# Kernel optimization log

Measured on AMD Instinct MI355X. Metric: run time of the kernel, lower is better.

Reference implementation:

```python
import jax, jax.numpy as jnp
import numpy as np

H, N, CH = 256, 64, 1  # heads/features, diagonal state size, channels


def setup_inputs() -> dict:
    key = jax.random.key(0)
    k1, k2, k3 = jax.random.split(key, 3)
    # |A| in (0.5, 0.999) so exp(dtA * l) decays for large l (matches rho*w construction)
    A_abslog = jnp.log(jax.random.uniform(k1, (H, N), dtype=jnp.float32,
                                          minval=0.5, maxval=0.999))
    A_phase = jax.random.uniform(k2, (H, N), dtype=jnp.float32,
                                 minval=-np.pi, maxval=np.pi)
    # C stored as real view of complex (channels, H, N, 2), like torch.view_as_real
    C = jax.random.normal(k3, (CH, H, N, 2), dtype=jnp.float32)
    return {"A_abslog": A_abslog, "A_phase": A_phase, "C": C, "L": 4096}


def reference(A_abslog, A_phase, C, L):
    # A_eigvals = exp(abslog + i*phase), copies=1 so repeat is identity
    A = jnp.exp(A_abslog + 1j * A_phase)            # (H, N) complex64
    dtA = jnp.log(A)                                 # (H, N)
    Cc = C[..., 0] + 1j * C[..., 1]                  # (CH, H, N)
    Cc = Cc * (A - 1.0) / dtA                        # (CH, H, N)
    t = jnp.arange(L, dtype=jnp.float32)             # (L,)
    K = jnp.exp(dtA[:, :, None] * t)                 # (H, N, L) Vandermonde
    K = jnp.einsum('chn,hnl->chl', Cc, K)            # (CH, H, L)
    return 2.0 * K.real
```

## Files before the change

### kernel.cpp

```cpp
#include <hip/hip_runtime.h>
#include <math.h>


typedef _Float16       f16x8 __attribute__((ext_vector_type(8)));
typedef unsigned int   u32x4 __attribute__((ext_vector_type(4)));
typedef float          f32x4 __attribute__((ext_vector_type(4)));

constexpr int H = 256;
constexpr int N = 64;
constexpr int L = 4096;
constexpr int STRIDE = 76;

constexpr unsigned SEL_LO = 0x05040100u;
constexpr unsigned SEL_HI = 0x07060302u;

__global__ __launch_bounds__(512)
void sskdiag_kernel(const float* __restrict__ A_abslog,
                    const float* __restrict__ A_phase,
                    const float* __restrict__ C,
                    float* __restrict__ out)
{
    __shared__ float4   s_t1[N];
    __shared__ float4   s_t2[N];
    __shared__ __align__(16) unsigned s_G[64 * STRIDE];
    __shared__ __align__(16) unsigned s_M[64 * STRIDE];

    const int h   = blockIdx.x;
    const int tid = threadIdx.x;

    if (tid < N) {
        const int n = tid;
        const float al = A_abslog[h * N + n];
        const float ph = A_phase [h * N + n];
        const double md = (double)ph * 0.15915494309189535;
        const float phrev = (float)(md - floor(md));
        const float sp = __builtin_amdgcn_sinf(phrev);
        const float cp = __builtin_amdgcn_cosf(phrev);
        const float m  = __expf(al);
        const float Ar = m * cp, Ai = m * sp;
        const float nr = Ar - 1.0f, ni = Ai;
        const float inv = 1.0f / (al * al + ph * ph);
        const float gr = (nr * al + ni * ph) * inv;
        const float gi = (ni * al - nr * ph) * inv;
        const float cre = C[(h * N + n) * 2 + 0];
        const float cim = C[(h * N + n) * 2 + 1];
        const float Cr = 2.0f * (cre * gr - cim * gi);
        const float Ci = 2.0f * (cre * gi + cim * gr);
        const double m64 = 64.0 * md;
        const float f64a = (float)(m64 - floor(m64));
        const float mg64 = __expf(64.0f * al);
        s_t1[n] = make_float4(al, phrev, Ar, Ai);
        s_t2[n] = make_float4(mg64 * __builtin_amdgcn_cosf(f64a),
                              mg64 * __builtin_amdgcn_sinf(f64a), Cr, Ci);
    }
    __syncthreads();

    {
        const int n = tid & 63, q = tid >> 6;
        const float4 t1 = s_t1[n];
        const float4 t2 = s_t2[n];
        const float al = t1.x, phrev = t1.y;
        const float Ar = t1.z, Ai = t1.w;
        const float Ur = t2.x, Ui = t2.y;
        const float b0 = (float)(8 * q);
        float tg = phrev * b0;  tg -= floorf(tg);
        const float gmag = __expf(al * b0);
        float gre = gmag * __builtin_amdgcn_cosf(tg);
        float gim = gmag * __builtin_amdgcn_sinf(tg);
        const float e0 = (float)(512 * q);
        float tm = phrev * e0;  tm -= floorf(tm);
        const float umag = __expf(al * e0);
        const float ure = umag * __builtin_amdgcn_cosf(tm);
        const float uim = umag * __builtin_amdgcn_sinf(tm);
        float mre = t2.z * ure - t2.w * uim;
        float mim = t2.z * uim + t2.w * ure;

        #pragma unroll
        for (int k = 0; k < 8; ++k) {
            const int row = 8 * q + k;
            union { _Float16 hh[2]; unsigned u; } pg, pm;
            pg.hh[0] = (_Float16)gre;  pg.hh[1] = (_Float16)(-gim);
            pm.hh[0] = (_Float16)mre;  pm.hh[1] = (_Float16)mim;
            s_G[row * STRIDE + n] = pg.u;
            s_M[row * STRIDE + n] = pm.u;
            const float ngr = gre * Ar - gim * Ai;
            gim = gre * Ai + gim * Ar;  gre = ngr;
            const float nmr = mre * Ur - mim * Ui;
            mim = mre * Ui + mim * Ur;  mre = nmr;
        }
    }
    __syncthreads();

    const int w    = tid >> 6;
    const int lane = tid & 63;
    const int e    = lane & 15;
    const int kg   = lane >> 4;
    const int ta   = w >> 1;
    const int tb0  = 2 * (w & 1);

    f16x8 fMr[2], fMi[2];
    #pragma unroll
    for (int s = 0; s < 2; ++s) {
        const unsigned* p = &s_M[(ta * 16 + e) * STRIDE + 32 * s + 8 * kg];
        const u32x4 v0 = *reinterpret_cast<const u32x4*>(p);
        const u32x4 v1 = *reinterpret_cast<const u32x4*>(p + 4);
        u32x4 rr, ii;
        rr[0] = __builtin_amdgcn_perm(v0[1], v0[0], SEL_LO);
        rr[1] = __builtin_amdgcn_perm(v0[3], v0[2], SEL_LO);
        rr[2] = __builtin_amdgcn_perm(v1[1], v1[0], SEL_LO);
        rr[3] = __builtin_amdgcn_perm(v1[3], v1[2], SEL_LO);
        ii[0] = __builtin_amdgcn_perm(v0[1], v0[0], SEL_HI);
        ii[1] = __builtin_amdgcn_perm(v0[3], v0[2], SEL_HI);
        ii[2] = __builtin_amdgcn_perm(v1[1], v1[0], SEL_HI);
        ii[3] = __builtin_amdgcn_perm(v1[3], v1[2], SEL_HI);
        fMr[s] = __builtin_bit_cast(f16x8, rr);
        fMi[s] = __builtin_bit_cast(f16x8, ii);
    }

    #pragma unroll
    for (int t = 0; t < 2; ++t) {
        const int tb = tb0 + t;
        f32x4 acc = {0.f, 0.f, 0.f, 0.f};
        #pragma unroll
        for (int s = 0; s < 2; ++s) {
            const unsigned* p = &s_G[(tb * 16 + e) * STRIDE + 32 * s + 8 * kg];
            const u32x4 v0 = *reinterpret_cast<const u32x4*>(p);
            const u32x4 v1 = *reinterpret_cast<const u32x4*>(p + 4);
            u32x4 rr, ii;
            rr[0] = __builtin_amdgcn_perm(v0[1], v0[0], SEL_LO);
            rr[1] = __builtin_amdgcn_perm(v0[3], v0[2], SEL_LO);
            rr[2] = __builtin_amdgcn_perm(v1[1], v1[0], SEL_LO);
            rr[3] = __builtin_amdgcn_perm(v1[3], v1[2], SEL_LO);
            ii[0] = __builtin_amdgcn_perm(v0[1], v0[0], SEL_HI);
            ii[1] = __builtin_amdgcn_perm(v0[3], v0[2], SEL_HI);
            ii[2] = __builtin_amdgcn_perm(v1[1], v1[0], SEL_HI);
            ii[3] = __builtin_amdgcn_perm(v1[3], v1[2], SEL_HI);
            const f16x8 fGr = __builtin_bit_cast(f16x8, rr);
            const f16x8 fGi = __builtin_bit_cast(f16x8, ii);
            acc = __builtin_amdgcn_mfma_f32_16x16x32_f16(fGr, fMr[s], acc, 0, 0, 0);
            acc = __builtin_amdgcn_mfma_f32_16x16x32_f16(fGi, fMi[s], acc, 0, 0, 0);
        }
        float4 v;
        v.x = acc[0];  v.y = acc[1];  v.z = acc[2];  v.w = acc[3];
        *reinterpret_cast<float4*>(out + h * L + (ta * 16 + e) * 64
                                   + tb * 16 + kg * 4) = v;
    }
}

extern "C" void kernel_launch(void* const* d_in, const int* in_sizes, int n_in,
                              void* d_out, int out_size, void* d_ws, size_t ws_size,
                              hipStream_t stream)
{
    const float* A_abslog = (const float*)d_in[0];
    const float* A_phase  = (const float*)d_in[1];
    const float* C        = (const float*)d_in[2];
    float* out = (float*)d_out;

    sskdiag_kernel<<<H, 512, 0, stream>>>(A_abslog, A_phase, C, out);
}
```

Baseline: 10.97 us.

## Halve block to 256 threads, each wave computing four output tiles

The block shrinks from 8 to 4 waves. Each thread now fills 16 rows of the G/M tables instead of 8. Each wave loads all four G tiles plus one M tile into registers and issues 16 MFMAs over four output tiles. The aim is to cut redundant LDS fragment loads and per-block thread overhead, at the cost of longer serial recurrence chains and fewer waves for latency hiding.

```diff
diff --git a/kernel.cpp b/kernel.cpp
--- a/kernel.cpp
+++ b/kernel.cpp
@@ -14,7 +14,7 @@
 constexpr unsigned SEL_LO = 0x05040100u;
 constexpr unsigned SEL_HI = 0x07060302u;
 
-__global__ __launch_bounds__(512)
+__global__ __launch_bounds__(256)
 void sskdiag_kernel(const float* __restrict__ A_abslog,
                     const float* __restrict__ A_phase,
                     const float* __restrict__ C,
@@ -62,22 +62,22 @@
         const float al = t1.x, phrev = t1.y;
         const float Ar = t1.z, Ai = t1.w;
         const float Ur = t2.x, Ui = t2.y;
-        const float b0 = (float)(8 * q);
+        const float b0 = (float)(16 * q);
         float tg = phrev * b0;  tg -= floorf(tg);
         const float gmag = __expf(al * b0);
         float gre = gmag * __builtin_amdgcn_cosf(tg);
         float gim = gmag * __builtin_amdgcn_sinf(tg);
-        const float e0 = (float)(512 * q);
-        float tm = phrev * e0;  tm -= floorf(tm);
-        const float umag = __expf(al * e0);
+        const float a64 = (float)(1024 * q);
+        float tm = phrev * a64;  tm -= floorf(tm);
+        const float umag = __expf(al * a64);
         const float ure = umag * __builtin_amdgcn_cosf(tm);
         const float uim = umag * __builtin_amdgcn_sinf(tm);
         float mre = t2.z * ure - t2.w * uim;
         float mim = t2.z * uim + t2.w * ure;
 
         #pragma unroll
-        for (int k = 0; k < 8; ++k) {
-            const int row = 8 * q + k;
+        for (int k = 0; k < 16; ++k) {
+            const int row = 16 * q + k;
             union { _Float16 hh[2]; unsigned u; } pg, pm;
             pg.hh[0] = (_Float16)gre;  pg.hh[1] = (_Float16)(-gim);
             pm.hh[0] = (_Float16)mre;  pm.hh[1] = (_Float16)mim;
@@ -95,34 +95,13 @@
     const int lane = tid & 63;
     const int e    = lane & 15;
     const int kg   = lane >> 4;
-    const int ta   = w >> 1;
-    const int tb0  = 2 * (w & 1);
 
-    f16x8 fMr[2], fMi[2];
+    f16x8 fGr[2][4], fGi[2][4], fMr[2], fMi[2];
+
     #pragma unroll
     for (int s = 0; s < 2; ++s) {
-        const unsigned* p = &s_M[(ta * 16 + e) * STRIDE + 32 * s + 8 * kg];
-        const u32x4 v0 = *reinterpret_cast<const u32x4*>(p);
-        const u32x4 v1 = *reinterpret_cast<const u32x4*>(p + 4);
-        u32x4 rr, ii;
-        rr[0] = __builtin_amdgcn_perm(v0[1], v0[0], SEL_LO);
-        rr[1] = __builtin_amdgcn_perm(v0[3], v0[2], SEL_LO);
-        rr[2] = __builtin_amdgcn_perm(v1[1], v1[0], SEL_LO);
-        rr[3] = __builtin_amdgcn_perm(v1[3], v1[2], SEL_LO);
-        ii[0] = __builtin_amdgcn_perm(v0[1], v0[0], SEL_HI);
-        ii[1] = __builtin_amdgcn_perm(v0[3], v0[2], SEL_HI);
-        ii[2] = __builtin_amdgcn_perm(v1[1], v1[0], SEL_HI);
-        ii[3] = __builtin_amdgcn_perm(v1[3], v1[2], SEL_HI);
-        fMr[s] = __builtin_bit_cast(f16x8, rr);
-        fMi[s] = __builtin_bit_cast(f16x8, ii);
-    }
-
-    #pragma unroll
-    for (int t = 0; t < 2; ++t) {
-        const int tb = tb0 + t;
-        f32x4 acc = {0.f, 0.f, 0.f, 0.f};
         #pragma unroll
-        for (int s = 0; s < 2; ++s) {
+        for (int tb = 0; tb < 4; ++tb) {
             const unsigned* p = &s_G[(tb * 16 + e) * STRIDE + 32 * s + 8 * kg];
             const u32x4 v0 = *reinterpret_cast<const u32x4*>(p);
             const u32x4 v1 = *reinterpret_cast<const u32x4*>(p + 4);
@@ -135,15 +114,39 @@
             ii[1] = __builtin_amdgcn_perm(v0[3], v0[2], SEL_HI);
             ii[2] = __builtin_amdgcn_perm(v1[1], v1[0], SEL_HI);
             ii[3] = __builtin_amdgcn_perm(v1[3], v1[2], SEL_HI);
-            const f16x8 fGr = __builtin_bit_cast(f16x8, rr);
-            const f16x8 fGi = __builtin_bit_cast(f16x8, ii);
-            acc = __builtin_amdgcn_mfma_f32_16x16x32_f16(fGr, fMr[s], acc, 0, 0, 0);
-            acc = __builtin_amdgcn_mfma_f32_16x16x32_f16(fGi, fMi[s], acc, 0, 0, 0);
+            fGr[s][tb] = __builtin_bit_cast(f16x8, rr);
+            fGi[s][tb] = __builtin_bit_cast(f16x8, ii);
         }
+        {
+            const unsigned* p = &s_M[(w * 16 + e) * STRIDE + 32 * s + 8 * kg];
+            const u32x4 v0 = *reinterpret_cast<const u32x4*>(p);
+            const u32x4 v1 = *reinterpret_cast<const u32x4*>(p + 4);
+            u32x4 rr, ii;
+            rr[0] = __builtin_amdgcn_perm(v0[1], v0[0], SEL_LO);
+            rr[1] = __builtin_amdgcn_perm(v0[3], v0[2], SEL_LO);
+            rr[2] = __builtin_amdgcn_perm(v1[1], v1[0], SEL_LO);
+            rr[3] = __builtin_amdgcn_perm(v1[3], v1[2], SEL_LO);
+            ii[0] = __builtin_amdgcn_perm(v0[1], v0[0], SEL_HI);
+            ii[1] = __builtin_amdgcn_perm(v0[3], v0[2], SEL_HI);
+            ii[2] = __builtin_amdgcn_perm(v1[1], v1[0], SEL_HI);
+            ii[3] = __builtin_amdgcn_perm(v1[3], v1[2], SEL_HI);
+            fMr[s] = __builtin_bit_cast(f16x8, rr);
+            fMi[s] = __builtin_bit_cast(f16x8, ii);
+        }
+    }
+
+    #pragma unroll
+    for (int tb = 0; tb < 4; ++tb) {
+        f32x4 acc = {0.f, 0.f, 0.f, 0.f};
+        #pragma unroll
+        for (int s = 0; s < 2; ++s) {
+            acc = __builtin_amdgcn_mfma_f32_16x16x32_f16(fGr[s][tb], fMr[s], acc, 0, 0, 0);
+            acc = __builtin_amdgcn_mfma_f32_16x16x32_f16(fGi[s][tb], fMi[s], acc, 0, 0, 0);
+        }
+        const int a = w * 16 + e;
         float4 v;
         v.x = acc[0];  v.y = acc[1];  v.z = acc[2];  v.w = acc[3];
-        *reinterpret_cast<float4*>(out + h * L + (ta * 16 + e) * 64
-                                   + tb * 16 + kg * 4) = v;
+        *reinterpret_cast<float4*>(out + h * L + a * 64 + tb * 16 + kg * 4) = v;
     }
 }
 
@@ -156,5 +159,5 @@
     const float* C        = (const float*)d_in[2];
     float* out = (float*)d_out;
 
-    sskdiag_kernel<<<H, 512, 0, stream>>>(A_abslog, A_phase, C, out);
+    sskdiag_kernel<<<H, 256, 0, stream>>>(A_abslog, A_phase, C, out);
 }
```

Result: faster. 9.798 us (-10.7%).
